# Optimization experiments

Hardware: AMD Instinct MI355X
Metric: run time of the kernel (lower is better)

The kernel has to match this reference:

```python
import jax, jax.numpy as jnp
import numpy as np

LEVEL_NUM = 8  # init kwarg level_num (scale is unused by forward)


def setup_inputs() -> dict:
    key = jax.random.key(0)
    x = jax.random.normal(key, (1, 1024, 1024), dtype=jnp.float32)
    return {"x": x}


def reference(x):
    N, H, W = x.shape
    L = LEVEL_NUM
    q_levels = jnp.linspace(x.min(), x.max(), L)          # (L,)
    sigma = 2.0 / L                                        # 1 / (level_num/2)
    # soft quantization: (N,H,W,L)
    quant = jnp.exp(-((x[..., None] - q_levels) ** 2) / (sigma ** 2))
    quant = jnp.transpose(quant, (0, 3, 1, 2))             # (N,L,H,W)
    quant = jnp.pad(quant, ((0, 0), (0, 0), (0, 1), (0, 1)))  # (N,L,H+1,W+1)
    quant_left = quant[:, :, None, :H, :W]                 # (N,L,1,H,W)
    quant_right = quant[:, None, :, 1:, 1:]                # (N,1,L,H,W)
    co_occurrence = quant_left * quant_right               # (N,L,L,H,W)
    sta = co_occurrence.sum(axis=(-1, -2))                 # (N,L,L)
    sta = sta / sta.sum(axis=(1, 2))                       # valid since N==1
    # q_levels_h[n,i,j] = q_levels[j]; q_levels_w[n,i,j] = q_levels[i]
    q_h = jnp.broadcast_to(q_levels[None, None, :], (N, L, L))
    q_w = jnp.broadcast_to(q_levels[None, :, None], (N, L, L))
    output = jnp.stack([q_h, q_w, sta], axis=1).reshape(N, 3, L * L)[0]  # (3, L*L)
    return output, quant[0], co_occurrence[0]
```

## Files before the change

### kernel.cpp

```cpp
#include <hip/hip_runtime.h>

#define H 1024
#define W 1024
#define L 8
#define QH 1025
#define QW 1025
#define OUT0 192
#define QUANT_ELEMS (L * QH * QW)

#define CROWS 32
#define NCHUNK 32
#define BPC 72

#define WS_MINP 0
#define WS_MAXP 256
#define WS_STA  512

__device__ __forceinline__ float qlev(float mn, float step, float mx, int i) {
    return (i == L - 1) ? mx : mn + step * (float)i;
}

__global__ __launch_bounds__(256) void k_minmax(const float4* __restrict__ x4,
                                                float* __restrict__ ws) {
    const int t = threadIdx.x, b = blockIdx.x;
    float mn = 1e30f, mx = -1e30f;
    #pragma unroll
    for (int i = 0; i < 4; ++i) {
        float4 v = x4[b * 1024 + i * 256 + t];
        mn = fminf(mn, fminf(fminf(v.x, v.y), fminf(v.z, v.w)));
        mx = fmaxf(mx, fmaxf(fmaxf(v.x, v.y), fmaxf(v.z, v.w)));
    }
    #pragma unroll
    for (int m = 1; m < 64; m <<= 1) {
        mn = fminf(mn, __shfl_xor(mn, m, 64));
        mx = fmaxf(mx, __shfl_xor(mx, m, 64));
    }
    __shared__ float smn[4], smx[4];
    if ((t & 63) == 0) { smn[t >> 6] = mn; smx[t >> 6] = mx; }
    __syncthreads();
    if (t == 0) {
        ws[WS_MINP + b] = fminf(fminf(smn[0], smn[1]), fminf(smn[2], smn[3]));
        ws[WS_MAXP + b] = fmaxf(fmaxf(smx[0], smx[1]), fmaxf(smx[2], smx[3]));
    }
}

__global__ __launch_bounds__(256) void k_main(const float* __restrict__ x,
                                              float* __restrict__ out,
                                              float* __restrict__ ws) {
    const int t = threadIdx.x;
    __shared__ float smn[4], smx[4], red[4];

    float mn = ws[WS_MINP + t], mx = ws[WS_MAXP + t];
    #pragma unroll
    for (int m = 1; m < 64; m <<= 1) {
        mn = fminf(mn, __shfl_xor(mn, m, 64));
        mx = fmaxf(mx, __shfl_xor(mx, m, 64));
    }
    if ((t & 63) == 0) { smn[t >> 6] = mn; smx[t >> 6] = mx; }
    __syncthreads();
    const float mnv = fminf(fminf(smn[0], smn[1]), fminf(smn[2], smn[3]));
    const float mxv = fmaxf(fmaxf(smx[0], smx[1]), fmaxf(smx[2], smx[3]));
    const float step = (mxv - mnv) * (1.0f / 7.0f);

    float* __restrict__ quant = out + OUT0;
    float* __restrict__ co    = out + OUT0 + QUANT_ELEMS;

    const int bid = blockIdx.x;
    const int c = bid / BPC, k = bid - c * BPC;
    const int r0 = c * CROWS;
    const int w0 = t * 4;
    const bool ok3 = (w0 + 4 < W);

    if (k < 64) {
        const float qi = qlev(mnv, step, mxv, k >> 3);
        const float qj = qlev(mnv, step, mxv, k & 7);
        float* cop = co + k * (H * W) + r0 * W + w0;
        float4 cur = *(const float4*)(x + r0 * W + w0);
        float acc = 0.0f;

        for (int r = 0; r < CROWS; ++r) {
            const int h = r0 + r;
            const bool hok = (h + 1 < H);
            float4 nxt = make_float4(0.f, 0.f, 0.f, 0.f);
            float e = 0.f;
            if (hok) {
                nxt = *(const float4*)(x + (h + 1) * W + w0);
                if (ok3) e = x[(h + 1) * W + w0 + 4];
            }
            float d;
            d = cur.x - qi; float l0 = __expf(-16.f * d * d);
            d = cur.y - qi; float l1 = __expf(-16.f * d * d);
            d = cur.z - qi; float l2 = __expf(-16.f * d * d);
            d = cur.w - qi; float l3 = __expf(-16.f * d * d);
            d = nxt.y - qj; float p0 = hok ? __expf(-16.f * d * d) : 0.f;
            d = nxt.z - qj; float p1 = hok ? __expf(-16.f * d * d) : 0.f;
            d = nxt.w - qj; float p2 = hok ? __expf(-16.f * d * d) : 0.f;
            d = e     - qj; float p3 = (hok && ok3) ? __expf(-16.f * d * d) : 0.f;

            float v0 = l0 * p0, v1 = l1 * p1, v2 = l2 * p2, v3 = l3 * p3;
            *(float4*)cop = make_float4(v0, v1, v2, v3);
            cop += W;
            acc += (v0 + v1) + (v2 + v3);
            cur = nxt;
        }

        #pragma unroll
        for (int m = 1; m < 64; m <<= 1) acc += __shfl_xor(acc, m, 64);
        if ((t & 63) == 0) red[t >> 6] = acc;
        __syncthreads();
        if (t == 0)
            ws[WS_STA + c * 64 + k] = (red[0] + red[1]) + (red[2] + red[3]);
    } else {
        const int i = k - 64;
        const float qi = qlev(mnv, step, mxv, i);
        for (int r = 0; r < CROWS; ++r) {
            const int h = r0 + r;
            float4 xl = *(const float4*)(x + h * W + w0);
            float d;
            d = xl.x - qi; float l0 = __expf(-16.f * d * d);
            d = xl.y - qi; float l1 = __expf(-16.f * d * d);
            d = xl.z - qi; float l2 = __expf(-16.f * d * d);
            d = xl.w - qi; float l3 = __expf(-16.f * d * d);
            float* row = quant + (i * QH + h) * QW + w0;
            *(float4*)row = make_float4(l0, l1, l2, l3);
            if (t == 255) row[4] = 0.0f;
        }
        if (c == NCHUNK - 1) {
            for (int w = t; w < QW; w += 256)
                quant[(i * QH + H) * QW + w] = 0.0f;
        }
    }
}

__global__ void k_final(float* __restrict__ out, const float* __restrict__ ws) {
    const int t = threadIdx.x;
    float mn = 1e30f, mx = -1e30f;
    #pragma unroll
    for (int i = 0; i < 4; ++i) {
        mn = fminf(mn, ws[WS_MINP + i * 64 + t]);
        mx = fmaxf(mx, ws[WS_MAXP + i * 64 + t]);
    }
    #pragma unroll
    for (int m = 1; m < 64; m <<= 1) {
        mn = fminf(mn, __shfl_xor(mn, m, 64));
        mx = fmaxf(mx, __shfl_xor(mx, m, 64));
    }
    const float step = (mx - mn) * (1.0f / 7.0f);

    float s = 0.f;
    #pragma unroll 8
    for (int c = 0; c < NCHUNK; ++c) s += ws[WS_STA + c * 64 + t];
    float tot = s;
    #pragma unroll
    for (int m = 1; m < 64; m <<= 1) tot += __shfl_xor(tot, m, 64);

    out[t]       = qlev(mn, step, mx, t & 7);
    out[64 + t]  = qlev(mn, step, mx, t >> 3);
    out[128 + t] = s / tot;
}

extern "C" void kernel_launch(void* const* d_in, const int* in_sizes, int n_in,
                              void* d_out, int out_size, void* d_ws, size_t ws_size,
                              hipStream_t stream) {
    const float* x = (const float*)d_in[0];
    float* out = (float*)d_out;
    float* ws = (float*)d_ws;

    k_minmax<<<dim3(256), dim3(256), 0, stream>>>((const float4*)x, ws);
    k_main<<<dim3(NCHUNK * BPC), dim3(256), 0, stream>>>(x, out, ws);
    k_final<<<dim3(1), dim3(64), 0, stream>>>(out, ws);
}
```

Baseline: 68.83 us.

## Compute all j co-occurrence planes per block reusing left quant and row loads

Each block now owns one left level i and a 16-row strip, and computes the quant plane plus all 8 co-occurrence planes for that i. This reuses the left exponentials, the quant write and the x loads across j instead of recomputing them in separate blocks. The grid shrinks to 512 blocks with an interleaving swizzle, and partial sums are reduced per j into a 64-unit workspace. The trade-off is fewer, longer blocks with 8 strided output streams each and more registers.

```diff
diff --git a/kernel.cpp b/kernel.cpp
--- a/kernel.cpp
+++ b/kernel.cpp
@@ -8,9 +8,8 @@
 #define OUT0 192
 #define QUANT_ELEMS (L * QH * QW)
 
-#define CROWS 32
-#define NCHUNK 32
-#define BPC 72
+#define UROWS 16
+#define NUNITS 512
 
 #define WS_MINP 0
 #define WS_MAXP 256
@@ -18,6 +17,10 @@
 
 __device__ __forceinline__ float qlev(float mn, float step, float mx, int i) {
     return (i == L - 1) ? mx : mn + step * (float)i;
+}
+__device__ __forceinline__ float ex16(float x, float q) {
+    float d = x - q;
+    return __expf(-16.f * d * d);
 }
 
 __global__ __launch_bounds__(256) void k_minmax(const float4* __restrict__ x4,
@@ -48,7 +51,8 @@
                                               float* __restrict__ out,
                                               float* __restrict__ ws) {
     const int t = threadIdx.x;
-    __shared__ float smn[4], smx[4], red[4];
+    __shared__ float smn[4], smx[4];
+    __shared__ float red[4][8];
 
     float mn = ws[WS_MINP + t], mx = ws[WS_MAXP + t];
     #pragma unroll
@@ -61,74 +65,84 @@
     const float mnv = fminf(fminf(smn[0], smn[1]), fminf(smn[2], smn[3]));
     const float mxv = fmaxf(fmaxf(smx[0], smx[1]), fmaxf(smx[2], smx[3]));
     const float step = (mxv - mnv) * (1.0f / 7.0f);
+    float qv[L];
+    #pragma unroll
+    for (int j = 0; j < L; ++j) qv[j] = qlev(mnv, step, mxv, j);
 
     float* __restrict__ quant = out + OUT0;
     float* __restrict__ co    = out + OUT0 + QUANT_ELEMS;
 
-    const int bid = blockIdx.x;
-    const int c = bid / BPC, k = bid - c * BPC;
-    const int r0 = c * CROWS;
+    const int sbid = (blockIdx.x & 7) * (NUNITS / 8) + (blockIdx.x >> 3);
+    const int c = sbid >> 4, i = (sbid >> 1) & 7, half = sbid & 1;
+    const int r0 = c * 32 + half * UROWS;
+    const float qi = qv[i];
+
     const int w0 = t * 4;
     const bool ok3 = (w0 + 4 < W);
 
-    if (k < 64) {
-        const float qi = qlev(mnv, step, mxv, k >> 3);
-        const float qj = qlev(mnv, step, mxv, k & 7);
-        float* cop = co + k * (H * W) + r0 * W + w0;
-        float4 cur = *(const float4*)(x + r0 * W + w0);
-        float acc = 0.0f;
+    float4 cur = *(const float4*)(x + r0 * W + w0);
+    float4 nxt = make_float4(0.f, 0.f, 0.f, 0.f);
+    float e = 0.f;
+    if (r0 + 1 < H) {
+        nxt = *(const float4*)(x + (r0 + 1) * W + w0);
+        if (ok3) e = x[(r0 + 1) * W + w0 + 4];
+    }
 
-        for (int r = 0; r < CROWS; ++r) {
-            const int h = r0 + r;
-            const bool hok = (h + 1 < H);
-            float4 nxt = make_float4(0.f, 0.f, 0.f, 0.f);
-            float e = 0.f;
-            if (hok) {
-                nxt = *(const float4*)(x + (h + 1) * W + w0);
-                if (ok3) e = x[(h + 1) * W + w0 + 4];
-            }
-            float d;
-            d = cur.x - qi; float l0 = __expf(-16.f * d * d);
-            d = cur.y - qi; float l1 = __expf(-16.f * d * d);
-            d = cur.z - qi; float l2 = __expf(-16.f * d * d);
-            d = cur.w - qi; float l3 = __expf(-16.f * d * d);
-            d = nxt.y - qj; float p0 = hok ? __expf(-16.f * d * d) : 0.f;
-            d = nxt.z - qj; float p1 = hok ? __expf(-16.f * d * d) : 0.f;
-            d = nxt.w - qj; float p2 = hok ? __expf(-16.f * d * d) : 0.f;
-            d = e     - qj; float p3 = (hok && ok3) ? __expf(-16.f * d * d) : 0.f;
+    float acc[L] = {0.f, 0.f, 0.f, 0.f, 0.f, 0.f, 0.f, 0.f};
 
-            float v0 = l0 * p0, v1 = l1 * p1, v2 = l2 * p2, v3 = l3 * p3;
-            *(float4*)cop = make_float4(v0, v1, v2, v3);
-            cop += W;
-            acc += (v0 + v1) + (v2 + v3);
-            cur = nxt;
+    for (int r = 0; r < UROWS; ++r) {
+        const int h = r0 + r;
+        float4 nx2 = make_float4(0.f, 0.f, 0.f, 0.f);
+        float e2 = 0.f;
+        if (h + 2 < H) {
+            nx2 = *(const float4*)(x + (h + 2) * W + w0);
+            if (ok3) e2 = x[(h + 2) * W + w0 + 4];
         }
 
+        float l0 = ex16(cur.x, qi), l1 = ex16(cur.y, qi),
+              l2 = ex16(cur.z, qi), l3 = ex16(cur.w, qi);
+        float* qp = quant + (i * QH + h) * QW + w0;
+        *(float4*)qp = make_float4(l0, l1, l2, l3);
+        if (t == 255) qp[4] = 0.0f;
+
+        float* cb = co + (i * L) * (H * W) + h * W + w0;
+        if (h + 1 < H) {
+            #pragma unroll
+            for (int j = 0; j < L; ++j) {
+                const float q = qv[j];
+                float p0 = ex16(nxt.y, q);
+                float p1 = ex16(nxt.z, q);
+                float p2 = ex16(nxt.w, q);
+                float p3 = ok3 ? ex16(e, q) : 0.f;
+                float v0 = l0 * p0, v1 = l1 * p1, v2 = l2 * p2, v3 = l3 * p3;
+                *(float4*)(cb + j * (H * W)) = make_float4(v0, v1, v2, v3);
+                acc[j] += (v0 + v1) + (v2 + v3);
+            }
+        } else {
+            #pragma unroll
+            for (int j = 0; j < L; ++j)
+                *(float4*)(cb + j * (H * W)) = make_float4(0.f, 0.f, 0.f, 0.f);
+        }
+
+        cur = nxt; nxt = nx2; e = e2;
+    }
+
+    if (c == NUNITS / 16 - 1 && half == 1) {
+        for (int w = t; w < QW; w += 256)
+            quant[(i * QH + H) * QW + w] = 0.0f;
+    }
+
+    #pragma unroll
+    for (int j = 0; j < L; ++j) {
+        float a = acc[j];
         #pragma unroll
-        for (int m = 1; m < 64; m <<= 1) acc += __shfl_xor(acc, m, 64);
-        if ((t & 63) == 0) red[t >> 6] = acc;
-        __syncthreads();
-        if (t == 0)
-            ws[WS_STA + c * 64 + k] = (red[0] + red[1]) + (red[2] + red[3]);
-    } else {
-        const int i = k - 64;
-        const float qi = qlev(mnv, step, mxv, i);
-        for (int r = 0; r < CROWS; ++r) {
-            const int h = r0 + r;
-            float4 xl = *(const float4*)(x + h * W + w0);
-            float d;
-            d = xl.x - qi; float l0 = __expf(-16.f * d * d);
-            d = xl.y - qi; float l1 = __expf(-16.f * d * d);
-            d = xl.z - qi; float l2 = __expf(-16.f * d * d);
-            d = xl.w - qi; float l3 = __expf(-16.f * d * d);
-            float* row = quant + (i * QH + h) * QW + w0;
-            *(float4*)row = make_float4(l0, l1, l2, l3);
-            if (t == 255) row[4] = 0.0f;
-        }
-        if (c == NCHUNK - 1) {
-            for (int w = t; w < QW; w += 256)
-                quant[(i * QH + H) * QW + w] = 0.0f;
-        }
+        for (int m = 1; m < 64; m <<= 1) a += __shfl_xor(a, m, 64);
+        if ((t & 63) == 0) red[t >> 6][j] = a;
+    }
+    __syncthreads();
+    if (t < L) {
+        float s = (red[0][t] + red[1][t]) + (red[2][t] + red[3][t]);
+        ws[WS_STA + (c * 2 + half) * 64 + i * 8 + t] = s;
     }
 }
 
@@ -149,7 +163,7 @@
 
     float s = 0.f;
     #pragma unroll 8
-    for (int c = 0; c < NCHUNK; ++c) s += ws[WS_STA + c * 64 + t];
+    for (int u = 0; u < 64; ++u) s += ws[WS_STA + u * 64 + t];
     float tot = s;
     #pragma unroll
     for (int m = 1; m < 64; m <<= 1) tot += __shfl_xor(tot, m, 64);
@@ -167,6 +181,6 @@
     float* ws = (float*)d_ws;
 
     k_minmax<<<dim3(256), dim3(256), 0, stream>>>((const float4*)x, ws);
-    k_main<<<dim3(NCHUNK * BPC), dim3(256), 0, stream>>>(x, out, ws);
+    k_main<<<dim3(NUNITS), dim3(256), 0, stream>>>(x, out, ws);
     k_final<<<dim3(1), dim3(64), 0, stream>>>(out, ws);
 }
```

Result: faster. 64.70 us (-6.0%).
